# Kernel tuning notes

Hardware: AMD Instinct MI355X
Metric: run time of the kernel (lower is better)

Reference implementation:

```python
import jax, jax.numpy as jnp
import numpy as np

TEMPERATURE = 0.07
EPS = 1e-8

def setup_inputs() -> dict:
    key = jax.random.key(0)
    k1, k2 = jax.random.split(key)
    features = jax.random.normal(k1, (8192, 512), dtype=jnp.float32)
    labels = jax.random.randint(k2, (8192,), 0, 100, dtype=jnp.int64)
    return {"features": features, "labels": labels}

def reference(features, labels):
    # L2-normalize rows (torch F.normalize uses eps=1e-12 clamp on norm)
    norm = jnp.maximum(jnp.linalg.norm(features, axis=1, keepdims=True), 1e-12)
    f = features / norm                                   # [B, D]
    sim = jnp.matmul(f, f.T) / TEMPERATURE                # [B, B]
    B = features.shape[0]
    same_label = (labels[:, None] == labels[None, :]).astype(features.dtype)
    diag = jnp.eye(B, dtype=bool)
    mask = jnp.where(diag, 0.0, same_label)               # positives, diag removed
    exp_sim = jnp.where(diag, 0.0, jnp.exp(sim))          # diag zeroed
    positive_sum = jnp.sum(exp_sim * mask, axis=1)        # [B]
    negative_sum = jnp.sum(exp_sim * (1.0 - mask), axis=1)
    loss = -jnp.log(positive_sum / (positive_sum + negative_sum + EPS))
    return loss.mean()
```

## Files before the change

kernel.cpp:

```cpp
#include <hip/hip_runtime.h>

#define BATCH 8192
#define DIM   512
#define NBLK  2080

typedef __attribute__((ext_vector_type(4))) int   int4v;
typedef __attribute__((ext_vector_type(8))) int   int8v;
typedef __attribute__((ext_vector_type(4))) float f32x4;
typedef unsigned char u8;

__device__ __forceinline__ void gload_lds16(const void* g, void* l){
  __builtin_amdgcn_global_load_lds(
      (const __attribute__((address_space(1))) void*)g,
      (__attribute__((address_space(3))) void*)l, 16, 0, 0);
}

template<int CTRL>
__device__ __forceinline__ float dpp_add(float v){
  int s = __builtin_amdgcn_update_dpp(0, __float_as_int(v), CTRL, 0xF, 0xF, true);
  return v + __int_as_float(s);
}
__device__ __forceinline__ float red16(float v){
  v = dpp_add<0xB1>(v);
  v = dpp_add<0x4E>(v);
  v = dpp_add<0x141>(v);
  v = dpp_add<0x140>(v);
  return v;
}

__device__ __forceinline__ u8 f2e4m3(float v){
  unsigned s = (__float_as_uint(v) >> 24) & 0x80u;
  float a = fabsf(v);
  if (a < 0.0009765625f) return (u8)s;
  if (a < 0.015625f){
    int qd = (int)rintf(a * 512.0f);
    return (u8)(s | (unsigned)qd);
  }
  unsigned u = __float_as_uint(a);
  int E = (int)(u >> 23) - 127;
  unsigned m = u & 0x7FFFFF;
  unsigned mant = m >> 20;
  unsigned rem  = m & 0xFFFFF;
  mant += (rem > 0x80000u || (rem == 0x80000u && (mant & 1u))) ? 1u : 0u;
  if (mant == 8u){ mant = 0u; E += 1; }
  return (u8)(s | ((unsigned)(E + 7) << 3) | mant);
}

__global__ __launch_bounds__(256) void k_normalize(const float* __restrict__ x,
                                                   u8* __restrict__ q){
  const int row  = blockIdx.x * 4 + (threadIdx.x >> 6);
  const int lane = threadIdx.x & 63;
  const float* xr = x + (size_t)row * DIM + lane * 8;
  float4 a = *(const float4*)xr;
  float4 b = *(const float4*)(xr + 4);
  float s = a.x*a.x + a.y*a.y + a.z*a.z + a.w*a.w
          + b.x*b.x + b.y*b.y + b.z*b.z + b.w*b.w;
  #pragma unroll
  for (int m = 1; m < 64; m <<= 1) s += __shfl_xor(s, m);
  const float inv = 1.0f / fmaxf(sqrtf(s), 1e-12f);
  float f[8] = {a.x, a.y, a.z, a.w, b.x, b.y, b.z, b.w};
  union { u8 b[8]; unsigned long long u; } pk;
  #pragma unroll
  for (int e = 0; e < 8; e++) pk.b[e] = f2e4m3(f[e] * inv);
  const int kb = lane >> 3;
  const int g  = lane & 7;
  const int sw = (row >> 1) & 3;
  const size_t off = (size_t)row * DIM + kb * 64
                   + (size_t)(((g >> 1) ^ sw) * 16 + (g & 1) * 8);
  *(unsigned long long*)(q + off) = pk.u;
}

__global__ __launch_bounds__(256, 3) void k_gemm(const u8* __restrict__ q,
                                                 const int* __restrict__ labels,
                                                 float* __restrict__ ppos,
                                                 float* __restrict__ ptot){
  __shared__ u8 sA[3][128 * 64];
  __shared__ u8 sB[3][128 * 64];
  __shared__ int labI[128], labJ[128];

  const int bid = (blockIdx.x & 7) * 260 + (blockIdx.x >> 3);
  int bj = (int)((sqrtf(8.0f * (float)bid + 1.0f) - 1.0f) * 0.5f);
  while ((bj + 1) * (bj + 2) / 2 <= bid) bj++;
  while (bj * (bj + 1) / 2 > bid) bj--;
  const int bi = bid - bj * (bj + 1) / 2;
  const bool mirror = (bi != bj);
  const int rowbase = bi * 128, colbase = bj * 128;

  const int t    = threadIdx.x;
  const int lane = t & 63;
  const int w    = t >> 6;
  const int wr   = w >> 1, wc = w & 1;
  const int lrow = lane & 15;
  const int g    = lane >> 4;
  const int bufsel = g >> 1;

  if (t < 128) labI[t] = labels[rowbase + t];
  else         labJ[t - 128] = labels[colbase + (t - 128)];

  const int sw = (lrow >> 1) & 3;
  const int ph = (((g & 1) * 2) ^ sw) * 16;
  int ra[4], rb[4];
  #pragma unroll
  for (int m = 0; m < 4; m++) ra[m] = (wr * 64 + m * 16 + lrow) * 64 + ph;
  #pragma unroll
  for (int n = 0; n < 4; n++) rb[n] = (wc * 64 + n * 16 + lrow) * 64 + ph;

  const u8* srcA = q + (size_t)(rowbase + (t >> 2)) * DIM + (t & 3) * 16;
  const u8* srcB = q + (size_t)(colbase + (t >> 2)) * DIM + (t & 3) * 16;
  const int dL = t * 16;

#define STAGE(BUF, KT) do{                                                \
    gload_lds16(srcA + (KT) * 64,             sA[BUF] + dL);              \
    gload_lds16(srcA + (KT) * 64 + 64 * DIM,  sA[BUF] + dL + 4096);       \
    gload_lds16(srcB + (KT) * 64,             sB[BUF] + dL);              \
    gload_lds16(srcB + (KT) * 64 + 64 * DIM,  sB[BUF] + dL + 4096);       \
  }while(0)

  f32x4 acc[4][4];
  #pragma unroll
  for (int m = 0; m < 4; m++)
    #pragma unroll
    for (int n = 0; n < 4; n++)
      acc[m][n] = (f32x4){0.f, 0.f, 0.f, 0.f};

  STAGE(0, 0);
  STAGE(1, 1);
  __syncthreads();

  #pragma unroll
  for (int u = 0; u < 4; ++u){
    const int b_lo = (2 * u) % 3;
    const int b_hi = (2 * u + 1) % 3;
    const int b_nx = (2 * u + 2) % 3;
    const u8* pA = bufsel ? sA[b_hi] : sA[b_lo];
    const u8* pB = bufsel ? sB[b_hi] : sB[b_lo];

    int8v av[4], bv[4];
    #pragma unroll
    for (int n = 0; n < 4; n++){
      int4v lo = *(const int4v*)(pB + rb[n]);
      int4v hi = *(const int4v*)(pB + (rb[n] ^ 16));
      bv[n] = __builtin_shufflevector(lo, hi, 0, 1, 2, 3, 4, 5, 6, 7);
    }
    #pragma unroll
    for (int m = 0; m < 4; m++){
      int4v lo = *(const int4v*)(pA + ra[m]);
      int4v hi = *(const int4v*)(pA + (ra[m] ^ 16));
      av[m] = __builtin_shufflevector(lo, hi, 0, 1, 2, 3, 4, 5, 6, 7);
    }
    __syncthreads();
    if (u < 3){ STAGE(b_nx, 2 * u + 2); STAGE(b_lo, 2 * u + 3); }
    __builtin_amdgcn_s_setprio(1);
    #pragma unroll
    for (int m = 0; m < 4; m++)
      #pragma unroll
      for (int n = 0; n < 4; n++)
        acc[m][n] = __builtin_amdgcn_mfma_scale_f32_16x16x128_f8f6f4(
            av[m], bv[n], acc[m][n], 0, 0, 0, 127, 0, 127);
    __builtin_amdgcn_s_setprio(0);
    __syncthreads();
  }
#undef STAGE

  const int i0 = rowbase + wr * 64;
  const int j0 = colbase + wc * 64;

  int lj_[4];
  #pragma unroll
  for (int n = 0; n < 4; n++)
    lj_[n] = labJ[wc * 64 + n * 16 + lrow];

  const float invT = 14.285714285714286f;
  #pragma unroll
  for (int m = 0; m < 4; m++)
    #pragma unroll
    for (int n = 0; n < 4; n++)
      #pragma unroll
      for (int e = 0; e < 4; e++){
        int i = i0 + m * 16 + g * 4 + e;
        int j = j0 + n * 16 + lrow;
        acc[m][n][e] = (i == j) ? 0.0f : __expf(acc[m][n][e] * invT);
      }

  {
    float* pp = ppos + (size_t)(2 * bj + wc) * BATCH;
    float* pt = ptot + (size_t)(2 * bj + wc) * BATCH;
    #pragma unroll
    for (int m = 0; m < 4; m++){
      int li4[4];
      #pragma unroll
      for (int e = 0; e < 4; e++) li4[e] = labI[wr * 64 + m * 16 + g * 4 + e];
      float tr[4] = {0, 0, 0, 0}, pr[4] = {0, 0, 0, 0};
      #pragma unroll
      for (int n = 0; n < 4; n++){
        int lj = lj_[n];
        #pragma unroll
        for (int e = 0; e < 4; e++){
          float v = acc[m][n][e];
          tr[e] += v;
          pr[e] += (li4[e] == lj) ? v : 0.0f;
        }
      }
      #pragma unroll
      for (int e = 0; e < 4; e++){
        tr[e] = red16(tr[e]);
        pr[e] = red16(pr[e]);
      }
      if (lrow == 0){
        int ib = i0 + m * 16 + g * 4;
        #pragma unroll
        for (int e = 0; e < 4; e++){
          pt[ib + e] = tr[e];
          pp[ib + e] = pr[e];
        }
      }
    }
  }

  if (mirror){
    float* pp = ppos + (size_t)(2 * bi + wr) * BATCH;
    float* pt = ptot + (size_t)(2 * bi + wr) * BATCH;
    #pragma unroll
    for (int n = 0; n < 4; n++){
      float ts = 0.f, ps = 0.f;
      int lj = lj_[n];
      #pragma unroll
      for (int m = 0; m < 4; m++){
        int li4[4];
        #pragma unroll
        for (int e = 0; e < 4; e++) li4[e] = labI[wr * 64 + m * 16 + g * 4 + e];
        #pragma unroll
        for (int e = 0; e < 4; e++){
          float v = acc[m][n][e];
          ts += v;
          ps += (li4[e] == lj) ? v : 0.0f;
        }
      }
      ts += __shfl_xor(ts, 16); ps += __shfl_xor(ps, 16);
      ts += __shfl_xor(ts, 32); ps += __shfl_xor(ps, 32);
      if (lane < 16){
        int j = j0 + n * 16 + lane;
        pt[j] = ts;
        pp[j] = ps;
      }
    }
  }
}

__global__ __launch_bounds__(256) void k_rowloss(const float* __restrict__ ppos,
                                                 const float* __restrict__ ptot,
                                                 float* __restrict__ bsum){
  __shared__ float sp[256], st2[256];
  const int t = threadIdx.x;
  const int r = blockIdx.x * 32 + (t & 31);
  const int c0 = t >> 5;
  float p = 0.f, tt = 0.f;
  for (int c = c0; c < 128; c += 8){
    p  += ppos[(size_t)c * BATCH + r];
    tt += ptot[(size_t)c * BATCH + r];
  }
  sp[t] = p; st2[t] = tt;
  __syncthreads();
  if (t < 32){
    float P = 0.f, T = 0.f;
    #pragma unroll
    for (int k = 0; k < 8; k++){ P += sp[t + k * 32]; T += st2[t + k * 32]; }
    sp[t] = -logf(P / (T + 1e-8f));
  }
  __syncthreads();
  if (t == 0){
    float s = 0.f;
    #pragma unroll
    for (int k = 0; k < 32; k++) s += sp[k];
    bsum[blockIdx.x] = s;
  }
}

__global__ __launch_bounds__(256) void k_final(const float* __restrict__ bsum,
                                               float* __restrict__ out){
  __shared__ float s4[4];
  float v = bsum[threadIdx.x];
  #pragma unroll
  for (int m = 1; m < 64; m <<= 1) v += __shfl_xor(v, m);
  if ((threadIdx.x & 63) == 0) s4[threadIdx.x >> 6] = v;
  __syncthreads();
  if (threadIdx.x == 0) out[0] = (s4[0] + s4[1] + s4[2] + s4[3]) * (1.0f / 8192.0f);
}

extern "C" void kernel_launch(void* const* d_in, const int* in_sizes, int n_in,
                              void* d_out, int out_size, void* d_ws, size_t ws_size,
                              hipStream_t stream){
  const float* x      = (const float*)d_in[0];
  const int*   labels = (const int*)d_in[1];
  float*       out    = (float*)d_out;

  char* ws = (char*)d_ws;
  u8*    q    = (u8*)ws;
  float* ppos = (float*)(ws + 8388608);
  float* ptot = (float*)(ws + 8388608 + 4194304);
  float* bsum = (float*)(ws + 8388608 + 8388608);

  k_normalize<<<BATCH / 4, 256, 0, stream>>>(x, q);
  k_gemm<<<NBLK, 256, 0, stream>>>(q, labels, ppos, ptot);
  k_rowloss<<<256, 256, 0, stream>>>(ppos, ptot, bsum);
  k_final<<<1, 256, 0, stream>>>(bsum, out);
}
```

Baseline: 66.22 us.

## Split B fragment loads around MFMAs and add per-k-block LDS swizzle

The main loop now loads all A fragments and only half the B fragments, issues the first half of the MFMAs, then loads the other B fragments before the barrier and staging. This is meant to overlap LDS reads with matrix work and cut B register pressure. The quantize kernel's swizzle also XORs in the k-block parity, and the GEMM read offset XORs in the buffer-select bit so both layouts agree, spreading LDS bank accesses across the two half-buffers. The risk is a wrong layout mapping giving incorrect results, or the split schedule adding stalls.

```diff
diff --git a/kernel.cpp b/kernel.cpp
--- a/kernel.cpp
+++ b/kernel.cpp
@@ -66,7 +66,7 @@
   const int g  = lane & 7;
   const int sw = (row >> 1) & 3;
   const size_t off = (size_t)row * DIM + kb * 64
-                   + (size_t)(((g >> 1) ^ sw) * 16 + (g & 1) * 8);
+                   + (size_t)((((g >> 1) ^ sw ^ (kb & 1)) & 3) * 16 + (g & 1) * 8);
   *(unsigned long long*)(q + off) = pk.u;
 }
 
@@ -98,7 +98,7 @@
   else         labJ[t - 128] = labels[colbase + (t - 128)];
 
   const int sw = (lrow >> 1) & 3;
-  const int ph = (((g & 1) * 2) ^ sw) * 16;
+  const int ph = ((((g & 1) * 2) ^ sw ^ bufsel) & 3) * 16;
   int ra[4], rb[4];
   #pragma unroll
   for (int m = 0; m < 4; m++) ra[m] = (wr * 64 + m * 16 + lrow) * 64 + ph;
@@ -115,6 +115,11 @@
     gload_lds16(srcB + (KT) * 64,             sB[BUF] + dL);              \
     gload_lds16(srcB + (KT) * 64 + 64 * DIM,  sB[BUF] + dL + 4096);       \
   }while(0)
+#define RD(DST, P, RO) do{                                                \
+    int4v lo_ = *(const int4v*)((P) + (RO));                              \
+    int4v hi_ = *(const int4v*)((P) + ((RO) ^ 16));                       \
+    DST = __builtin_shufflevector(lo_, hi_, 0, 1, 2, 3, 4, 5, 6, 7);      \
+  }while(0)
 
   f32x4 acc[4][4];
   #pragma unroll
@@ -135,32 +140,35 @@
     const u8* pA = bufsel ? sA[b_hi] : sA[b_lo];
     const u8* pB = bufsel ? sB[b_hi] : sB[b_lo];
 
-    int8v av[4], bv[4];
-    #pragma unroll
-    for (int n = 0; n < 4; n++){
-      int4v lo = *(const int4v*)(pB + rb[n]);
-      int4v hi = *(const int4v*)(pB + (rb[n] ^ 16));
-      bv[n] = __builtin_shufflevector(lo, hi, 0, 1, 2, 3, 4, 5, 6, 7);
-    }
-    #pragma unroll
-    for (int m = 0; m < 4; m++){
-      int4v lo = *(const int4v*)(pA + ra[m]);
-      int4v hi = *(const int4v*)(pA + (ra[m] ^ 16));
-      av[m] = __builtin_shufflevector(lo, hi, 0, 1, 2, 3, 4, 5, 6, 7);
-    }
+    int8v av[4], bvx[2];
+    #pragma unroll
+    for (int m = 0; m < 4; m++) RD(av[m], pA, ra[m]);
+    #pragma unroll
+    for (int n = 0; n < 2; n++) RD(bvx[n], pB, rb[n]);
+    __builtin_amdgcn_s_setprio(1);
+    #pragma unroll
+    for (int m = 0; m < 4; m++)
+      #pragma unroll
+      for (int n = 0; n < 2; n++)
+        acc[m][n] = __builtin_amdgcn_mfma_scale_f32_16x16x128_f8f6f4(
+            av[m], bvx[n], acc[m][n], 0, 0, 0, 127, 0, 127);
+    __builtin_amdgcn_s_setprio(0);
+    #pragma unroll
+    for (int n = 0; n < 2; n++) RD(bvx[n], pB, rb[2 + n]);
     __syncthreads();
     if (u < 3){ STAGE(b_nx, 2 * u + 2); STAGE(b_lo, 2 * u + 3); }
     __builtin_amdgcn_s_setprio(1);
     #pragma unroll
     for (int m = 0; m < 4; m++)
       #pragma unroll
-      for (int n = 0; n < 4; n++)
-        acc[m][n] = __builtin_amdgcn_mfma_scale_f32_16x16x128_f8f6f4(
-            av[m], bv[n], acc[m][n], 0, 0, 0, 127, 0, 127);
+      for (int n = 0; n < 2; n++)
+        acc[m][2 + n] = __builtin_amdgcn_mfma_scale_f32_16x16x128_f8f6f4(
+            av[m], bvx[n], acc[m][2 + n], 0, 0, 0, 127, 0, 127);
     __builtin_amdgcn_s_setprio(0);
     __syncthreads();
   }
 #undef STAGE
+#undef RD
 
   const int i0 = rowbase + wr * 64;
   const int j0 = colbase + wc * 64;
```

Result: slower. 71.45 us (+7.9%).
